# Optimization experiments

Measured on AMD Instinct MI355X. Metric: run time of the kernel, lower is better.

The kernel has to match this reference:

```python
import jax, jax.numpy as jnp
import numpy as np

B, L, D = 2, 2048, 2048
H, KV, HD = 16, 4, 64  # query heads, kv heads, head_dim
EPS = 1e-6
ROPE_BASE = 10000.0


def setup_inputs() -> dict:
    key = jax.random.key(0)
    k0, k1, k2 = jax.random.split(key, 3)
    x = jax.random.normal(k0, (B, L, D), dtype=jnp.float32)
    W_qkv = jax.random.normal(k1, ((H + 2 * KV) * HD, D), dtype=jnp.float32) * 0.02
    W_out = jax.random.normal(k2, (D, H * HD), dtype=jnp.float32) * 0.02
    q_norm_w = jnp.ones((HD,), dtype=jnp.float32)
    k_norm_w = jnp.ones((HD,), dtype=jnp.float32)
    # causal additive mask (forward's optional `mask` arg)
    mask = jnp.triu(jnp.full((L, L), -1e9, dtype=jnp.float32), k=1)
    return {"x": x, "W_qkv": W_qkv, "W_out": W_out,
            "q_norm_w": q_norm_w, "k_norm_w": k_norm_w, "mask": mask}


def _rms_norm(x, w):
    # normalize over last (head) dim
    var = jnp.mean(x * x, axis=-1, keepdims=True)
    return x * jax.lax.rsqrt(var + EPS) * w


def _rope(x):
    # x: [B, nH, L, HD]; non-traditional (rotate-half) RoPE, offset=0
    half = HD // 2
    freqs = ROPE_BASE ** (-jnp.arange(0, HD, 2, dtype=jnp.float32) / HD)  # [half]
    theta = jnp.arange(L, dtype=jnp.float32)[:, None] * freqs[None, :]    # [L, half]
    cos, sin = jnp.cos(theta), jnp.sin(theta)
    x1, x2 = x[..., :half], x[..., half:]
    return jnp.concatenate([x1 * cos - x2 * sin, x1 * sin + x2 * cos], axis=-1)


def reference(x, W_qkv, W_out, q_norm_w, k_norm_w, mask):
    # fused QKV projection
    qkv = jnp.einsum("bld,ed->ble", x, W_qkv)                       # [B,L,(H+2KV)*HD]
    qkv = qkv.reshape(B, L, H + 2 * KV, HD).transpose(0, 2, 1, 3)   # [B,nH,L,HD]
    q, k, v = jnp.split(qkv, [H, H + KV], axis=1)
    # per-head QK RMSNorm + RoPE
    q = _rope(_rms_norm(q, q_norm_w))
    k = _rope(_rms_norm(k, k_norm_w))
    # GQA: repeat kv heads to match query heads
    rep = H // KV
    k = jnp.repeat(k, rep, axis=1)
    v = jnp.repeat(v, rep, axis=1)
    scale = HD ** -0.5
    scores = jnp.einsum("bhqd,bhkd->bhqk", q, k) * scale + mask      # [B,H,L,L]
    attn = jax.nn.softmax(scores, axis=-1)
    out = jnp.einsum("bhqk,bhkd->bhqd", attn, v)                     # [B,H,L,HD]
    out = out.transpose(0, 2, 1, 3).reshape(B, L, H * HD)
    return jnp.einsum("ble,de->bld", out, W_out)                     # [B,L,D]
```

## Files before the change

### kernel.cpp

```cpp
#include <hip/hip_runtime.h>
#include <hip/hip_bf16.h>


typedef __bf16 bf16;
typedef bf16 bf16x8 __attribute__((ext_vector_type(8)));
typedef bf16 bf16x4 __attribute__((ext_vector_type(4)));
typedef float f32x4 __attribute__((ext_vector_type(4)));

#define L_SEQ 2048
#define NQH 16
#define NKVH 4

typedef __attribute__((address_space(3))) void lds_void;
typedef const __attribute__((address_space(1))) void glb_void;
__device__ __forceinline__ void async_ld16(const void* g, void* l) {
  __builtin_amdgcn_global_load_lds((glb_void*)g, (lds_void*)l, 16, 0, 0);
}

__global__ __launch_bounds__(256) void cast_bf16(const float* __restrict__ in,
                                                 bf16* __restrict__ out, int n) {
  int i = (blockIdx.x * 256 + threadIdx.x) * 4;
  if (i < n) {
    float4 v = *(const float4*)&in[i];
    bf16x4 o;
    o[0] = (bf16)v.x; o[1] = (bf16)v.y; o[2] = (bf16)v.z; o[3] = (bf16)v.w;
    *(bf16x4*)&out[i] = o;
  }
}

template <int BN>
__global__ __launch_bounds__(256)
void gemm_bt(const bf16* __restrict__ A, const bf16* __restrict__ B,
             float* __restrict__ C, int M, int N, int K) {
  constexpr int ASZ = 128 * 32, BSZ = BN * 32;
  constexpr int BI = BN / 64;
  constexpr int NJ = BN / 32;
  __shared__ bf16 As[2 * ASZ];
  __shared__ bf16 Bs[2 * BSZ];
  const int tid = threadIdx.x;
  const int lane = tid & 63, w = tid >> 6;
  const int lq = lane & 15, g = lane >> 4;
  const int wr = w >> 1, wc = w & 1;
  const int bx = blockIdx.x, by = blockIdx.y;

  const bf16* gA[2];
  bf16* ldsA[2];
  const bf16* gB[BI];
  bf16* ldsB[BI];
#pragma unroll
  for (int c = 0; c < 2; ++c) {
    int slot = c * 256 + tid;
    int row = slot >> 2, ch = slot & 3;
    int sch = ch ^ ((row >> 1) & 3);
    gA[c] = &A[(size_t)(by * 128 + row) * K + sch * 8];
    ldsA[c] = &As[(c * 256 + w * 64) * 8];
  }
#pragma unroll
  for (int c = 0; c < BI; ++c) {
    int slot = c * 256 + tid;
    int row = slot >> 2, ch = slot & 3;
    int sch = ch ^ ((row >> 1) & 3);
    gB[c] = &B[(size_t)(bx * BN + row) * K + sch * 8];
    ldsB[c] = &Bs[(c * 256 + w * 64) * 8];
  }

  auto stage = [&](int kt, int buf) {
#pragma unroll
    for (int c = 0; c < 2; ++c) async_ld16(gA[c] + kt * 32, ldsA[c] + buf * ASZ);
#pragma unroll
    for (int c = 0; c < BI; ++c) async_ld16(gB[c] + kt * 32, ldsB[c] + buf * BSZ);
  };

  f32x4 acc[4][NJ] = {};
  const int nk = K >> 5;
  int cur = 0;

  stage(0, 0);
  __syncthreads();
  for (int kt = 0; kt < nk; ++kt) {
    bf16x8 af[4], bfr[NJ];
#pragma unroll
    for (int i = 0; i < 4; ++i) {
      int ra = wr * 64 + i * 16 + lq;
      af[i] = *(const bf16x8*)&As[cur * ASZ + ra * 32 + (g ^ ((ra >> 1) & 3)) * 8];
    }
#pragma unroll
    for (int j = 0; j < NJ; ++j) {
      int rb = wc * (BN / 2) + j * 16 + lq;
      bfr[j] = *(const bf16x8*)&Bs[cur * BSZ + rb * 32 + (g ^ ((rb >> 1) & 3)) * 8];
    }
    if (kt + 1 < nk) stage(kt + 1, cur ^ 1);
#pragma unroll
    for (int i = 0; i < 4; ++i)
#pragma unroll
      for (int j = 0; j < NJ; ++j)
        acc[i][j] = __builtin_amdgcn_mfma_f32_16x16x32_bf16(af[i], bfr[j], acc[i][j], 0, 0, 0);
    __syncthreads();
    cur ^= 1;
  }
#pragma unroll
  for (int i = 0; i < 4; ++i)
#pragma unroll
    for (int j = 0; j < NJ; ++j) {
      int row = by * 128 + wr * 64 + i * 16 + g * 4;
      int col = bx * BN + wc * (BN / 2) + j * 16 + lq;
#pragma unroll
      for (int r = 0; r < 4; ++r) C[(size_t)(row + r) * N + col] = acc[i][j][r];
    }
}

__global__ __launch_bounds__(256)
void norm_rope(const float* __restrict__ qkv, const float* __restrict__ qw,
               const float* __restrict__ kw, bf16* __restrict__ Qb,
               bf16* __restrict__ Kb, bf16* __restrict__ Vb) {
  const int bl = blockIdx.x;
  const int b = bl >> 11, l = bl & (L_SEQ - 1);
  const int w = threadIdx.x >> 6, lane = threadIdx.x & 63;
  const int i = lane & 31;
  float freq = exp2f(-(float)i * 0.41524101186280154f);
  float theta = (float)l * freq;
  float sn, cs;
  sincosf(theta, &sn, &cs);
  float qwl = qw[lane], kwl = kw[lane];

  for (int h = w; h < 24; h += 4) {
    float v = qkv[(size_t)bl * 1536 + h * 64 + lane];
    if (h < 20) {
      float ss = v * v;
#pragma unroll
      for (int off = 32; off; off >>= 1) ss += __shfl_xor(ss, off);
      float rs = rsqrtf(ss * (1.f / 64.f) + 1e-6f);
      float wt = (h < 16) ? qwl : kwl;
      float y = v * rs * wt;
      float part = __shfl_xor(y, 32);
      float out = (lane < 32) ? (y * cs - part * sn) : (part * sn + y * cs);
      if (h < 16)
        Qb[((size_t)(b * NQH + h) * L_SEQ + l) * 64 + lane] = (bf16)(out * 0.125f);
      else
        Kb[((size_t)(b * NKVH + (h - 16)) * L_SEQ + l) * 64 + lane] = (bf16)out;
    } else {
      Vb[((size_t)(b * NKVH + (h - 20)) * L_SEQ + l) * 64 + lane] = (bf16)v;
    }
  }
}

__global__ __launch_bounds__(256)
void transpose_v(const bf16* __restrict__ Vb, bf16* __restrict__ Vt) {
  __shared__ bf16 T[64 * 66];
  const int bk = blockIdx.y;
  const int l0 = blockIdx.x * 64;
  const int t = threadIdx.x;
  const bf16* src = Vb + (size_t)bk * L_SEQ * 64;
#pragma unroll
  for (int c = 0; c < 2; ++c) {
    int idx = c * 256 + t;
    int row = idx >> 3, ch = idx & 7;
    bf16x8 v = *(const bf16x8*)&src[(size_t)(l0 + row) * 64 + ch * 8];
#pragma unroll
    for (int j = 0; j < 8; ++j) T[(ch * 8 + j) * 66 + row] = v[j];
  }
  __syncthreads();
  bf16* dst = Vt + (size_t)bk * 64 * L_SEQ;
#pragma unroll
  for (int c = 0; c < 2; ++c) {
    int idx = c * 256 + t;
    int d = idx >> 3, ch = idx & 7;
    bf16x8 v;
#pragma unroll
    for (int j = 0; j < 8; ++j) v[j] = T[d * 66 + ch * 8 + j];
    *(bf16x8*)&dst[(size_t)d * L_SEQ + l0 + ch * 8] = v;
  }
}

__global__ __launch_bounds__(256)
void attn(const bf16* __restrict__ Qb, const bf16* __restrict__ Kb,
          const bf16* __restrict__ Vt, bf16* __restrict__ Ao) {
  const int pair = blockIdx.x;
  const int bh = blockIdx.y;
  const int b = bh >> 4, h = bh & 15, kv = h >> 2;
  const int tid = threadIdx.x;
  const int w = tid >> 6, lane = tid & 63;
  const int lq = lane & 15, g = lane >> 4;

  __shared__ bf16 Ks[64][64];
  __shared__ bf16 Vs[64][64];
  __shared__ bf16 Plds[4][16][72];

  const bf16* Qp = Qb + (size_t)(b * NQH + h) * L_SEQ * 64;
  const bf16* Kp = Kb + (size_t)(b * NKVH + kv) * L_SEQ * 64;
  const bf16* Vp = Vt + (size_t)(b * NKVH + kv) * 64 * L_SEQ;

  const int sr0 = tid >> 3, sc = tid & 7;
  const int sr1 = sr0 + 32;
  const int swc0 = (sc ^ (sr0 & 7)) * 8;
  bf16x8 rk0, rk1, rv0, rv1;

  auto load_tile = [&](int k0) {
    rk0 = *(const bf16x8*)&Kp[(size_t)(k0 + sr0) * 64 + sc * 8];
    rk1 = *(const bf16x8*)&Kp[(size_t)(k0 + sr1) * 64 + sc * 8];
    rv0 = *(const bf16x8*)&Vp[(size_t)sr0 * L_SEQ + k0 + sc * 8];
    rv1 = *(const bf16x8*)&Vp[(size_t)sr1 * L_SEQ + k0 + sc * 8];
  };
  auto write_tile = [&]() {
    *(bf16x8*)&Ks[sr0][swc0] = rk0;
    *(bf16x8*)&Ks[sr1][swc0] = rk1;
    *(bf16x8*)&Vs[sr0][swc0] = rv0;
    *(bf16x8*)&Vs[sr1][swc0] = rv1;
  };

  const float L2E = 1.4426950408889634f;

  for (int half = 0; half < 2; ++half) {
    const int qblk = half ? (31 - pair) : pair;
    const int qr0 = qblk * 64 + w * 16;
    const int qg = qr0 + lq;

    bf16x8 qf[2];
    qf[0] = *(const bf16x8*)&Qp[(qr0 + lq) * 64 + g * 8];
    qf[1] = *(const bf16x8*)&Qp[(qr0 + lq) * 64 + 32 + g * 8];

    f32x4 o[4] = {};
    float m = -1e30f, lsum = 0.f;

    const int nkt = qblk + 1;
    load_tile(0);
    __syncthreads();
    write_tile();
    __syncthreads();

    for (int kt = 0; kt < nkt; ++kt) {
      const int k0 = kt * 64;
      const bool diag = (kt == nkt - 1);
      if (kt + 1 < nkt) load_tile(k0 + 64);

      f32x4 s[4] = {};
#pragma unroll
      for (int ks = 0; ks < 4; ++ks) {
        if (!diag || ks <= w) {
          const int row = ks * 16 + lq, sw = lq & 7;
          bf16x8 kf0 = *(const bf16x8*)&Ks[row][(g ^ sw) * 8];
          bf16x8 kf1 = *(const bf16x8*)&Ks[row][((g + 4) ^ sw) * 8];
          s[ks] = __builtin_amdgcn_mfma_f32_16x16x32_bf16(kf0, qf[0], s[ks], 0, 0, 0);
          s[ks] = __builtin_amdgcn_mfma_f32_16x16x32_bf16(kf1, qf[1], s[ks], 0, 0, 0);
        }
      }
      if (diag) {
#pragma unroll
        for (int ks = 0; ks < 4; ++ks)
#pragma unroll
          for (int r = 0; r < 4; ++r)
            if (k0 + ks * 16 + g * 4 + r > qg) s[ks][r] = -1e30f;
      }
      float tmax = -1e30f;
#pragma unroll
      for (int ks = 0; ks < 4; ++ks)
#pragma unroll
        for (int r = 0; r < 4; ++r) tmax = fmaxf(tmax, s[ks][r]);
      tmax = fmaxf(tmax, __shfl_xor(tmax, 16));
      tmax = fmaxf(tmax, __shfl_xor(tmax, 32));
      float mnew = fmaxf(m, tmax);
      float alpha = exp2f((m - mnew) * L2E);
      m = mnew;
      float rsum = 0.f;
#pragma unroll
      for (int ks = 0; ks < 4; ++ks) {
        bf16x4 p;
#pragma unroll
        for (int r = 0; r < 4; ++r) {
          float pv = exp2f((s[ks][r] - mnew) * L2E);
          rsum += pv;
          p[r] = (bf16)pv;
        }
        *(bf16x4*)&Plds[w][lq][ks * 16 + g * 4] = p;
      }
      rsum += __shfl_xor(rsum, 16);
      rsum += __shfl_xor(rsum, 32);
      lsum = lsum * alpha + rsum;

      float ar[4];
#pragma unroll
      for (int r = 0; r < 4; ++r) ar[r] = __shfl(alpha, (lane & 48) | (g * 4 + r));
#pragma unroll
      for (int dt = 0; dt < 4; ++dt)
#pragma unroll
        for (int r = 0; r < 4; ++r) o[dt][r] *= ar[r];

      bf16x8 pf0 = *(const bf16x8*)&Plds[w][lq][g * 8];
      bf16x8 pf1 = *(const bf16x8*)&Plds[w][lq][32 + g * 8];
#pragma unroll
      for (int dt = 0; dt < 4; ++dt) {
        const int row = dt * 16 + lq, sw = lq & 7;
        bf16x8 vf0 = *(const bf16x8*)&Vs[row][(g ^ sw) * 8];
        o[dt] = __builtin_amdgcn_mfma_f32_16x16x32_bf16(pf0, vf0, o[dt], 0, 0, 0);
        if (!diag || w >= 2) {
          bf16x8 vf1 = *(const bf16x8*)&Vs[row][((g + 4) ^ sw) * 8];
          o[dt] = __builtin_amdgcn_mfma_f32_16x16x32_bf16(pf1, vf1, o[dt], 0, 0, 0);
        }
      }

      if (kt + 1 < nkt) {
        __syncthreads();
        write_tile();
        __syncthreads();
      }
    }

    float linv = 1.f / lsum;
#pragma unroll
    for (int r = 0; r < 4; ++r) {
      float li = __shfl(linv, (lane & 48) | (g * 4 + r));
      int row = b * L_SEQ + qr0 + g * 4 + r;
#pragma unroll
      for (int dt = 0; dt < 4; ++dt)
        Ao[(size_t)row * 1024 + h * 64 + dt * 16 + lq] = (bf16)(o[dt][r] * li);
    }
  }
}

extern "C" void kernel_launch(void* const* d_in, const int* in_sizes, int n_in,
                              void* d_out, int out_size, void* d_ws, size_t ws_size,
                              hipStream_t stream) {
  const float* x = (const float*)d_in[0];
  const float* Wqkv = (const float*)d_in[1];
  const float* Wout = (const float*)d_in[2];
  const float* qw = (const float*)d_in[3];
  const float* kw = (const float*)d_in[4];
  float* out = (float*)d_out;

  char* ws = (char*)d_ws;
  size_t off = 0;
  auto alloc = [&](size_t bytes) {
    void* p = ws + off;
    off = (off + bytes + 255) & ~(size_t)255;
    return p;
  };
  bf16* xb = (bf16*)alloc(8388608ull * 2);
  bf16* wqb = (bf16*)alloc(3145728ull * 2);
  bf16* wob = (bf16*)alloc(2097152ull * 2);
  float* qkv = (float*)alloc(4096ull * 1536 * 4);
  bf16* Qb = (bf16*)alloc(4194304ull * 2);
  bf16* Kb = (bf16*)alloc(1048576ull * 2);
  bf16* Vb = (bf16*)alloc(1048576ull * 2);
  bf16* Vt = (bf16*)alloc(1048576ull * 2);
  bf16* Ao = (bf16*)alloc(4194304ull * 2);

  cast_bf16<<<8192, 256, 0, stream>>>(x, xb, 8388608);
  cast_bf16<<<3072, 256, 0, stream>>>(Wqkv, wqb, 3145728);
  cast_bf16<<<2048, 256, 0, stream>>>(Wout, wob, 2097152);
  gemm_bt<64><<<dim3(24, 32), 256, 0, stream>>>(xb, wqb, qkv, 4096, 1536, 2048);
  norm_rope<<<4096, 256, 0, stream>>>(qkv, qw, kw, Qb, Kb, Vb);
  transpose_v<<<dim3(32, 8), 256, 0, stream>>>(Vb, Vt);
  attn<<<dim3(16, 32), 256, 0, stream>>>(Qb, Kb, Vt, Ao);
  gemm_bt<128><<<dim3(16, 32), 256, 0, stream>>>(Ao, wob, out, 4096, 2048, 1024);
}
```

Baseline: 271.2 us.

## Fuse QKV GEMM epilogue with RMSNorm, RoPE and V transpose

The QKV projection GEMM now stages its output tile in shared memory and applies per-head RMSNorm and RoPE in the epilogue. It writes Q/K directly as bf16, and for V heads writes the transposed layout. This removes the fp32 qkv intermediate round trip and two kernel launches (norm_rope, transpose_v). The output projection also switches from a 128-wide to a 64-wide N tile with more blocks. The cost is recomputing sincos per element in the epilogue and using a larger dynamic shared-memory allocation.

```diff
diff --git a/kernel.cpp b/kernel.cpp
--- a/kernel.cpp
+++ b/kernel.cpp
@@ -28,13 +28,11 @@
   }
 }
 
-template <int BN>
+
 __global__ __launch_bounds__(256)
-void gemm_bt(const bf16* __restrict__ A, const bf16* __restrict__ B,
-             float* __restrict__ C, int M, int N, int K) {
-  constexpr int ASZ = 128 * 32, BSZ = BN * 32;
-  constexpr int BI = BN / 64;
-  constexpr int NJ = BN / 32;
+void gemm_bt64(const bf16* __restrict__ A, const bf16* __restrict__ B,
+               float* __restrict__ C, int M, int N, int K) {
+  constexpr int ASZ = 128 * 32, BSZ = 64 * 32;
   __shared__ bf16 As[2 * ASZ];
   __shared__ bf16 Bs[2 * BSZ];
   const int tid = threadIdx.x;
@@ -45,8 +43,8 @@
 
   const bf16* gA[2];
   bf16* ldsA[2];
-  const bf16* gB[BI];
-  bf16* ldsB[BI];
+  const bf16* gB0;
+  bf16* ldsB0;
 #pragma unroll
   for (int c = 0; c < 2; ++c) {
     int slot = c * 256 + tid;
@@ -55,120 +53,184 @@
     gA[c] = &A[(size_t)(by * 128 + row) * K + sch * 8];
     ldsA[c] = &As[(c * 256 + w * 64) * 8];
   }
-#pragma unroll
-  for (int c = 0; c < BI; ++c) {
+  {
+    int row = tid >> 2, ch = tid & 3;
+    int sch = ch ^ ((row >> 1) & 3);
+    gB0 = &B[(size_t)(bx * 64 + row) * K + sch * 8];
+    ldsB0 = &Bs[(w * 64) * 8];
+  }
+
+  f32x4 acc[4][2] = {};
+  const int nk = K >> 5;
+  int cur = 0;
+
+#pragma unroll
+  for (int c = 0; c < 2; ++c) async_ld16(gA[c], ldsA[c]);
+  async_ld16(gB0, ldsB0);
+  __syncthreads();
+  for (int kt = 0; kt < nk; ++kt) {
+    bf16x8 af[4], bfr[2];
+#pragma unroll
+    for (int i = 0; i < 4; ++i) {
+      int ra = wr * 64 + i * 16 + lq;
+      af[i] = *(const bf16x8*)&As[cur * ASZ + ra * 32 + (g ^ ((ra >> 1) & 3)) * 8];
+    }
+#pragma unroll
+    for (int j = 0; j < 2; ++j) {
+      int rb = wc * 32 + j * 16 + lq;
+      bfr[j] = *(const bf16x8*)&Bs[cur * BSZ + rb * 32 + (g ^ ((rb >> 1) & 3)) * 8];
+    }
+    if (kt + 1 < nk) {
+#pragma unroll
+      for (int c = 0; c < 2; ++c) async_ld16(gA[c] + (kt + 1) * 32, ldsA[c] + (cur ^ 1) * ASZ);
+      async_ld16(gB0 + (kt + 1) * 32, ldsB0 + (cur ^ 1) * BSZ);
+    }
+#pragma unroll
+    for (int i = 0; i < 4; ++i)
+#pragma unroll
+      for (int j = 0; j < 2; ++j)
+        acc[i][j] = __builtin_amdgcn_mfma_f32_16x16x32_bf16(af[i], bfr[j], acc[i][j], 0, 0, 0);
+    __syncthreads();
+    cur ^= 1;
+  }
+#pragma unroll
+  for (int i = 0; i < 4; ++i)
+#pragma unroll
+    for (int j = 0; j < 2; ++j) {
+      int row = by * 128 + wr * 64 + i * 16 + g * 4;
+      int col = bx * 64 + wc * 32 + j * 16 + lq;
+#pragma unroll
+      for (int r = 0; r < 4; ++r) C[(size_t)(row + r) * N + col] = acc[i][j][r];
+    }
+}
+
+__global__ __launch_bounds__(256)
+void gemm_qkv_fused(const bf16* __restrict__ A, const bf16* __restrict__ B,
+                    const float* __restrict__ qw, const float* __restrict__ kw,
+                    bf16* __restrict__ Qb, bf16* __restrict__ Kb,
+                    bf16* __restrict__ Vt) {
+  constexpr int K = 2048;
+  constexpr int ASZ = 128 * 32, BSZ = 64 * 32;
+  extern __shared__ char smem[];
+  bf16* As = (bf16*)smem;
+  bf16* Bs = (bf16*)(smem + 2 * ASZ * 2);
+  float* F = (float*)smem;
+  const int tid = threadIdx.x;
+  const int lane = tid & 63, w = tid >> 6;
+  const int lq = lane & 15, g = lane >> 4;
+  const int wr = w >> 1, wc = w & 1;
+  const int bx = blockIdx.x, by = blockIdx.y;
+
+  const bf16* gA[2];
+  bf16* ldsA[2];
+  const bf16* gB0;
+  bf16* ldsB0;
+#pragma unroll
+  for (int c = 0; c < 2; ++c) {
     int slot = c * 256 + tid;
     int row = slot >> 2, ch = slot & 3;
     int sch = ch ^ ((row >> 1) & 3);
-    gB[c] = &B[(size_t)(bx * BN + row) * K + sch * 8];
-    ldsB[c] = &Bs[(c * 256 + w * 64) * 8];
-  }
-
-  auto stage = [&](int kt, int buf) {
-#pragma unroll
-    for (int c = 0; c < 2; ++c) async_ld16(gA[c] + kt * 32, ldsA[c] + buf * ASZ);
-#pragma unroll
-    for (int c = 0; c < BI; ++c) async_ld16(gB[c] + kt * 32, ldsB[c] + buf * BSZ);
-  };
-
-  f32x4 acc[4][NJ] = {};
-  const int nk = K >> 5;
+    gA[c] = &A[(size_t)(by * 128 + row) * K + sch * 8];
+    ldsA[c] = &As[(c * 256 + w * 64) * 8];
+  }
+  {
+    int row = tid >> 2, ch = tid & 3;
+    int sch = ch ^ ((row >> 1) & 3);
+    gB0 = &B[(size_t)(bx * 64 + row) * K + sch * 8];
+    ldsB0 = &Bs[(w * 64) * 8];
+  }
+
+  f32x4 acc[4][2] = {};
+  constexpr int nk = K >> 5;
   int cur = 0;
 
-  stage(0, 0);
+#pragma unroll
+  for (int c = 0; c < 2; ++c) async_ld16(gA[c], ldsA[c]);
+  async_ld16(gB0, ldsB0);
   __syncthreads();
   for (int kt = 0; kt < nk; ++kt) {
-    bf16x8 af[4], bfr[NJ];
+    bf16x8 af[4], bfr[2];
 #pragma unroll
     for (int i = 0; i < 4; ++i) {
       int ra = wr * 64 + i * 16 + lq;
       af[i] = *(const bf16x8*)&As[cur * ASZ + ra * 32 + (g ^ ((ra >> 1) & 3)) * 8];
     }
 #pragma unroll
-    for (int j = 0; j < NJ; ++j) {
-      int rb = wc * (BN / 2) + j * 16 + lq;
+    for (int j = 0; j < 2; ++j) {
+      int rb = wc * 32 + j * 16 + lq;
       bfr[j] = *(const bf16x8*)&Bs[cur * BSZ + rb * 32 + (g ^ ((rb >> 1) & 3)) * 8];
     }
-    if (kt + 1 < nk) stage(kt + 1, cur ^ 1);
+    if (kt + 1 < nk) {
+#pragma unroll
+      for (int c = 0; c < 2; ++c) async_ld16(gA[c] + (kt + 1) * 32, ldsA[c] + (cur ^ 1) * ASZ);
+      async_ld16(gB0 + (kt + 1) * 32, ldsB0 + (cur ^ 1) * BSZ);
+    }
 #pragma unroll
     for (int i = 0; i < 4; ++i)
 #pragma unroll
-      for (int j = 0; j < NJ; ++j)
+      for (int j = 0; j < 2; ++j)
         acc[i][j] = __builtin_amdgcn_mfma_f32_16x16x32_bf16(af[i], bfr[j], acc[i][j], 0, 0, 0);
     __syncthreads();
     cur ^= 1;
   }
+
 #pragma unroll
   for (int i = 0; i < 4; ++i)
 #pragma unroll
-    for (int j = 0; j < NJ; ++j) {
-      int row = by * 128 + wr * 64 + i * 16 + g * 4;
-      int col = bx * BN + wc * (BN / 2) + j * 16 + lq;
-#pragma unroll
-      for (int r = 0; r < 4; ++r) C[(size_t)(row + r) * N + col] = acc[i][j][r];
-    }
-}
-
-__global__ __launch_bounds__(256)
-void norm_rope(const float* __restrict__ qkv, const float* __restrict__ qw,
-               const float* __restrict__ kw, bf16* __restrict__ Qb,
-               bf16* __restrict__ Kb, bf16* __restrict__ Vb) {
-  const int bl = blockIdx.x;
-  const int b = bl >> 11, l = bl & (L_SEQ - 1);
-  const int w = threadIdx.x >> 6, lane = threadIdx.x & 63;
-  const int i = lane & 31;
-  float freq = exp2f(-(float)i * 0.41524101186280154f);
-  float theta = (float)l * freq;
-  float sn, cs;
-  sincosf(theta, &sn, &cs);
-  float qwl = qw[lane], kwl = kw[lane];
-
-  for (int h = w; h < 24; h += 4) {
-    float v = qkv[(size_t)bl * 1536 + h * 64 + lane];
-    if (h < 20) {
-      float ss = v * v;
-#pragma unroll
-      for (int off = 32; off; off >>= 1) ss += __shfl_xor(ss, off);
-      float rs = rsqrtf(ss * (1.f / 64.f) + 1e-6f);
-      float wt = (h < 16) ? qwl : kwl;
-      float y = v * rs * wt;
-      float part = __shfl_xor(y, 32);
-      float out = (lane < 32) ? (y * cs - part * sn) : (part * sn + y * cs);
-      if (h < 16)
-        Qb[((size_t)(b * NQH + h) * L_SEQ + l) * 64 + lane] = (bf16)(out * 0.125f);
-      else
-        Kb[((size_t)(b * NKVH + (h - 16)) * L_SEQ + l) * 64 + lane] = (bf16)out;
-    } else {
-      Vb[((size_t)(b * NKVH + (h - 20)) * L_SEQ + l) * 64 + lane] = (bf16)v;
-    }
-  }
-}
-
-__global__ __launch_bounds__(256)
-void transpose_v(const bf16* __restrict__ Vb, bf16* __restrict__ Vt) {
-  __shared__ bf16 T[64 * 66];
-  const int bk = blockIdx.y;
-  const int l0 = blockIdx.x * 64;
-  const int t = threadIdx.x;
-  const bf16* src = Vb + (size_t)bk * L_SEQ * 64;
-#pragma unroll
-  for (int c = 0; c < 2; ++c) {
-    int idx = c * 256 + t;
-    int row = idx >> 3, ch = idx & 7;
-    bf16x8 v = *(const bf16x8*)&src[(size_t)(l0 + row) * 64 + ch * 8];
-#pragma unroll
-    for (int j = 0; j < 8; ++j) T[(ch * 8 + j) * 66 + row] = v[j];
-  }
+    for (int j = 0; j < 2; ++j) {
+      int row = wr * 64 + i * 16 + g * 4;
+      int col = wc * 32 + j * 16 + lq;
+#pragma unroll
+      for (int r = 0; r < 4; ++r) F[(row + r) * 66 + col] = acc[i][j][r];
+    }
   __syncthreads();
-  bf16* dst = Vt + (size_t)bk * 64 * L_SEQ;
-#pragma unroll
-  for (int c = 0; c < 2; ++c) {
-    int idx = c * 256 + t;
-    int d = idx >> 3, ch = idx & 7;
-    bf16x8 v;
-#pragma unroll
-    for (int j = 0; j < 8; ++j) v[j] = T[d * 66 + ch * 8 + j];
-    *(bf16x8*)&dst[(size_t)d * L_SEQ + l0 + ch * 8] = v;
+
+  const int h = bx;
+  const int b = by >> 4;
+  const int l0 = (by & 15) * 128;
+
+  if (h < 20) {
+    const int row = tid >> 1;
+    const int half = tid & 1;
+    const float* Fr = &F[row * 66];
+    float ss = 0.f;
+#pragma unroll
+    for (int c = 0; c < 32; ++c) {
+      float v = Fr[half * 32 + c];
+      ss += v * v;
+    }
+    ss += __shfl_xor(ss, 1);
+    const float rs = rsqrtf(ss * (1.f / 64.f) + 1e-6f);
+    const int l = l0 + row;
+    const float* wn = (h < 16) ? qw : kw;
+    const float scale = (h < 16) ? 0.125f : 1.f;
+    bf16 lo[16], hi[16];
+#pragma unroll
+    for (int k = 0; k < 16; ++k) {
+      int c = half * 16 + k;
+      float x1 = Fr[c] * rs * wn[c];
+      float x2 = Fr[c + 32] * rs * wn[c + 32];
+      float theta = (float)l * exp2f(-(float)c * 0.41524101186280154f);
+      float sn, cs;
+      sincosf(theta, &sn, &cs);
+      lo[k] = (bf16)((x1 * cs - x2 * sn) * scale);
+      hi[k] = (bf16)((x1 * sn + x2 * cs) * scale);
+    }
+    bf16* dst = (h < 16) ? &Qb[((size_t)(b * NQH + h) * L_SEQ + l) * 64]
+                         : &Kb[((size_t)(b * NKVH + (h - 16)) * L_SEQ + l) * 64];
+    *(bf16x8*)&dst[half * 16] = *(bf16x8*)&lo[0];
+    *(bf16x8*)&dst[half * 16 + 8] = *(bf16x8*)&lo[8];
+    *(bf16x8*)&dst[half * 16 + 32] = *(bf16x8*)&hi[0];
+    *(bf16x8*)&dst[half * 16 + 40] = *(bf16x8*)&hi[8];
+  } else {
+    const int d = tid >> 2;
+    const int lg = (tid & 3) * 32;
+    bf16 tv[32];
+#pragma unroll
+    for (int jj = 0; jj < 32; ++jj) tv[jj] = (bf16)F[(lg + jj) * 66 + d];
+    bf16* dst = &Vt[(size_t)(b * NKVH + (h - 20)) * 64 * L_SEQ + (size_t)d * L_SEQ + l0 + lg];
+#pragma unroll
+    for (int c = 0; c < 4; ++c) *(bf16x8*)&dst[c * 8] = *(bf16x8*)&tv[c * 8];
   }
 }
 
@@ -337,19 +399,15 @@
   bf16* xb = (bf16*)alloc(8388608ull * 2);
   bf16* wqb = (bf16*)alloc(3145728ull * 2);
   bf16* wob = (bf16*)alloc(2097152ull * 2);
-  float* qkv = (float*)alloc(4096ull * 1536 * 4);
   bf16* Qb = (bf16*)alloc(4194304ull * 2);
   bf16* Kb = (bf16*)alloc(1048576ull * 2);
-  bf16* Vb = (bf16*)alloc(1048576ull * 2);
   bf16* Vt = (bf16*)alloc(1048576ull * 2);
   bf16* Ao = (bf16*)alloc(4194304ull * 2);
 
   cast_bf16<<<8192, 256, 0, stream>>>(x, xb, 8388608);
   cast_bf16<<<3072, 256, 0, stream>>>(Wqkv, wqb, 3145728);
   cast_bf16<<<2048, 256, 0, stream>>>(Wout, wob, 2097152);
-  gemm_bt<64><<<dim3(24, 32), 256, 0, stream>>>(xb, wqb, qkv, 4096, 1536, 2048);
-  norm_rope<<<4096, 256, 0, stream>>>(qkv, qw, kw, Qb, Kb, Vb);
-  transpose_v<<<dim3(32, 8), 256, 0, stream>>>(Vb, Vt);
+  gemm_qkv_fused<<<dim3(24, 32), 256, 33792, stream>>>(xb, wqb, qw, kw, Qb, Kb, Vt);
   attn<<<dim3(16, 32), 256, 0, stream>>>(Qb, Kb, Vt, Ao);
-  gemm_bt<128><<<dim3(16, 32), 256, 0, stream>>>(Ao, wob, out, 4096, 2048, 1024);
-}
+  gemm_bt64<<<dim3(32, 32), 256, 0, stream>>>(Ao, wob, out, 4096, 2048, 1024);
+}
```

Measured after the change: 271.9 us. No clear change (+0.3%).
